# Performance work log

Hardware: AMD Instinct MI355X
Metric: run time of the kernel (lower is better)

## Reference

```python
import jax, jax.numpy as jnp
import numpy as np

B, S = 1, 2048
H, KV, D = 32, 8, 128          # query heads, kv heads, head_size
G = H // KV                     # num_queries_per_kv (GQA group size)
SCALE = 1.0 / float(np.sqrt(D))


def setup_inputs() -> dict:
    key = jax.random.key(0)
    k1, k2, k3 = jax.random.split(key, 3)
    slopes = jnp.asarray(2.0 ** (-8.0 * np.arange(1, H + 1) / H), dtype=jnp.float32)
    return {
        "query": jax.random.normal(k1, (B, S, H * D), dtype=jnp.float32),
        "key": jax.random.normal(k2, (B, S, KV * D), dtype=jnp.float32),
        "value": jax.random.normal(k3, (B, S, KV * D), dtype=jnp.float32),
        "alibi_slopes": slopes,
    }


def reference(query, key, value, alibi_slopes):
    b, s, _ = query.shape
    # [B,S,H*D] -> [B,KV,G,S,D] (GQA unflatten of query heads into kv groups)
    q = query.reshape(b, s, KV, G, D).transpose(0, 2, 3, 1, 4)
    k = key.reshape(b, s, KV, D).transpose(0, 2, 1, 3)      # [B,KV,S,D]
    v = value.reshape(b, s, KV, D).transpose(0, 2, 1, 3)    # [B,KV,S,D]

    # _make_alibi_bias: bias[i,j] = (j - i) * slope_h, then unflatten heads to (KV, G)
    pos = jnp.arange(s)
    rel = (pos[None, :] - pos[:, None]).astype(query.dtype)         # [S,S]
    bias = alibi_slopes[:, None, None] * rel                        # [H,S,S]
    causal = jnp.where(pos[None, :] > pos[:, None], -jnp.inf, 0.0).astype(query.dtype)
    bias = (bias + causal).reshape(KV, G, s, s)                     # [KV,G,S,S]

    # scaled QK^T + bias, softmax, AV (non-fused prompt_attention path)
    scores = jnp.einsum('bkgsd,bktd->bkgst', q * SCALE, k) + bias   # [B,KV,G,S,S]
    probs = jax.nn.softmax(scores, axis=-1)
    out = jnp.einsum('bkgst,bktd->bkgsd', probs, v)                 # [B,KV,G,S,D]
    # flatten (KV,G) -> H and back to [B,S,H*D]
    return out.transpose(0, 3, 1, 2, 4).reshape(b, s, H * D)
```

## Files before the change

kernel.cpp:

```cpp
#include <hip/hip_runtime.h>
#include <hip/hip_bf16.h>

#define S_LEN 2048
#define NHEADS 32
#define NKV 8
#define HD 128
#define QK_SCALE 0.08838834764831845f
#define LOG2E 1.4426950408889634f
#define QK_SCALE2 (QK_SCALE * LOG2E)
#define DTHR 11.5416f

#define BQ 64
#define BK 32
#define NQT (S_LEN / BQ)
#define QSTR (NHEADS * HD)
#define KSTR (NKV * HD)

#define K_STRIDE 136
#define VT_STRIDE 40

typedef __attribute__((ext_vector_type(8))) short bf16x8;
typedef __attribute__((ext_vector_type(4))) float f32x4;
typedef __attribute__((ext_vector_type(4))) unsigned u32x4;

__device__ inline unsigned cvt_pk_bf16(float lo, float hi) {
    unsigned r;
    asm("v_cvt_pk_bf16_f32 %0, %1, %2" : "=v"(r) : "v"(lo), "v"(hi));
    return r;
}
__device__ inline bf16x8 as_bf16x8(u32x4 v) {
    union { u32x4 u; bf16x8 b; } c; c.u = v; return c.b;
}

__global__ __launch_bounds__(256) void attn_fwd(
    const float* __restrict__ Q, const float* __restrict__ K,
    const float* __restrict__ V, const float* __restrict__ SL,
    float* __restrict__ O)
{
    const int bx   = blockIdx.x;
    const int h    = bx & (NHEADS - 1);
    const int qt   = (NQT - 1) - (bx >> 5);
    const int kvh  = h >> 2;
    const float slope  = SL[h];
    const float slope2 = slope * LOG2E;

    const int tid  = threadIdx.x;
    const int lane = tid & 63;
    const int w    = tid >> 6;
    const int l16  = lane & 15;
    const int lq   = lane >> 4;

    __shared__ short Ks[2][BK * K_STRIDE];
    __shared__ short VTs[2][HD * VT_STRIDE];

    const int qrow0 = qt * BQ + w * 16;
    const int q     = qrow0 + l16;

    bf16x8 qf[4];
    {
        const float* qp = Q + (size_t)q * QSTR + h * HD + lq * 8;
        #pragma unroll
        for (int d0 = 0; d0 < 4; ++d0) {
            f32x4 a = *(const f32x4*)(qp + d0 * 32);
            f32x4 b = *(const f32x4*)(qp + d0 * 32 + 4);
            u32x4 t;
            t[0] = cvt_pk_bf16(a[0] * QK_SCALE2, a[1] * QK_SCALE2);
            t[1] = cvt_pk_bf16(a[2] * QK_SCALE2, a[3] * QK_SCALE2);
            t[2] = cvt_pk_bf16(b[0] * QK_SCALE2, b[1] * QK_SCALE2);
            t[3] = cvt_pk_bf16(b[2] * QK_SCALE2, b[3] * QK_SCALE2);
            qf[d0] = as_bf16x8(t);
        }
    }

    f32x4 acc[8];
    #pragma unroll
    for (int t = 0; t < 8; ++t) acc[t] = (f32x4){0.f, 0.f, 0.f, 0.f};
    float m_ = -1e30f, l_ = 0.f;

    const int kv_end = qt * BQ + BQ;
    int kb_start = 0;
    {
        float th = (float)(qt * BQ) - 31.0f - 45.0f / slope;
        int t = (int)floorf(th);
        kb_start = (t < 0) ? 0 : (((t >> 5) + 1) << 5);
    }

    const int sr  = tid >> 4, scc = tid & 15;
    const int vd  = tid & 127, vrb = (tid >> 7) * 8;
    const float* Kbase = K + (size_t)kvh * HD + scc * 8;
    const float* Vbase = V + (size_t)kvh * HD + vd;

    float kr[2][8], vr[2][8];

    auto load_regs = [&](int kb) {
        #pragma unroll
        for (int s = 0; s < 2; ++s) {
            const float* kp = Kbase + (size_t)(kb + sr + s * 16) * KSTR;
            *(f32x4*)&kr[s][0] = *(const f32x4*)kp;
            *(f32x4*)&kr[s][4] = *(const f32x4*)(kp + 4);
        }
        #pragma unroll
        for (int s = 0; s < 2; ++s)
            #pragma unroll
            for (int j = 0; j < 8; ++j)
                vr[s][j] = Vbase[(size_t)(kb + vrb + s * 16 + j) * KSTR];
    };

    auto store_tile = [&](int b) {
        #pragma unroll
        for (int s = 0; s < 2; ++s) {
            u32x4 t;
            t[0] = cvt_pk_bf16(kr[s][0], kr[s][1]);
            t[1] = cvt_pk_bf16(kr[s][2], kr[s][3]);
            t[2] = cvt_pk_bf16(kr[s][4], kr[s][5]);
            t[3] = cvt_pk_bf16(kr[s][6], kr[s][7]);
            *(u32x4*)&Ks[b][(sr + s * 16) * K_STRIDE + scc * 8] = t;
        }
        #pragma unroll
        for (int s = 0; s < 2; ++s) {
            u32x4 t;
            t[0] = cvt_pk_bf16(vr[s][0], vr[s][1]);
            t[1] = cvt_pk_bf16(vr[s][2], vr[s][3]);
            t[2] = cvt_pk_bf16(vr[s][4], vr[s][5]);
            t[3] = cvt_pk_bf16(vr[s][6], vr[s][7]);
            *(u32x4*)&VTs[b][vd * VT_STRIDE + vrb + s * 16] = t;
        }
    };

    load_regs(kb_start);
    store_tile(0);
    int cur = 0;

    const int srcA = l16 + ((lane & 16) << 1);
    const int srcB = srcA + 16;
    const bool lowk = (lq < 2);

    for (int kb = kb_start; kb < kv_end; kb += BK) {
        asm volatile("s_waitcnt lgkmcnt(0)\n\ts_barrier" ::: "memory");

        const bool has_next = (kb + BK) < kv_end;
        if (has_next) load_regs(kb + BK);

        const bool live = (kb <= qrow0 + 15) &&
                          (slope * (float)(qrow0 - kb - 31) < 45.0f);
        if (live) {
            const short* Kc = &Ks[cur][0];
            const short* Vc = &VTs[cur][0];

            f32x4 sc0 = (f32x4){0.f,0.f,0.f,0.f};
            f32x4 sc1 = (f32x4){0.f,0.f,0.f,0.f};
            #pragma unroll
            for (int d0 = 0; d0 < 4; ++d0) {
                bf16x8 kf0 = *(const bf16x8*)&Kc[l16 * K_STRIDE + d0 * 32 + lq * 8];
                bf16x8 kf1 = *(const bf16x8*)&Kc[(16 + l16) * K_STRIDE + d0 * 32 + lq * 8];
                sc0 = __builtin_amdgcn_mfma_f32_16x16x32_bf16(kf0, qf[d0], sc0, 0, 0, 0);
                sc1 = __builtin_amdgcn_mfma_f32_16x16x32_bf16(kf1, qf[d0], sc1, 0, 0, 0);
            }

            const int kq0 = kb + 4 * lq - q;
            float s[8];
            #pragma unroll
            for (int i = 0; i < 4; ++i) {
                int d0i = kq0 + i, d1i = kq0 + 16 + i;
                float b0 = __builtin_fmaf(slope2, (float)d0i, sc0[i]);
                float b1 = __builtin_fmaf(slope2, (float)d1i, sc1[i]);
                s[i]     = (d0i > 0) ? -1e30f : b0;
                s[i + 4] = (d1i > 0) ? -1e30f : b1;
            }

            float rm = fmaxf(fmaxf(fmaxf(s[0], s[1]), fmaxf(s[2], s[3])),
                             fmaxf(fmaxf(s[4], s[5]), fmaxf(s[6], s[7])));
            rm = fmaxf(rm, __shfl_xor(rm, 16));
            rm = fmaxf(rm, __shfl_xor(rm, 32));

            bool need = (rm > m_ + DTHR);
            if (__any(need)) {
                float mn    = need ? rm : m_;
                float alpha = exp2f(m_ - mn);
                m_ = mn;
                l_ *= alpha;
                #pragma unroll
                for (int t = 0; t < 8; ++t) {
                    acc[t][0] *= alpha; acc[t][1] *= alpha;
                    acc[t][2] *= alpha; acc[t][3] *= alpha;
                }
            }

            float p[8];
            #pragma unroll
            for (int j = 0; j < 8; ++j) p[j] = exp2f(s[j] - m_);
            float ts = ((p[0] + p[1]) + (p[2] + p[3])) +
                       ((p[4] + p[5]) + (p[6] + p[7]));
            ts += __shfl_xor(ts, 16);
            ts += __shfl_xor(ts, 32);
            l_ += ts;

            unsigned t0 = cvt_pk_bf16(p[0], p[1]);
            unsigned t1 = cvt_pk_bf16(p[2], p[3]);
            unsigned t2 = cvt_pk_bf16(p[4], p[5]);
            unsigned t3 = cvt_pk_bf16(p[6], p[7]);
            unsigned a0 = __shfl(t0, srcA), c0 = __shfl(t2, srcA);
            unsigned a1 = __shfl(t1, srcA), c1 = __shfl(t3, srcA);
            unsigned a2 = __shfl(t0, srcB), c2 = __shfl(t2, srcB);
            unsigned a3 = __shfl(t1, srcB), c3 = __shfl(t3, srcB);
            u32x4 Bf;
            Bf[0] = lowk ? a0 : c0;
            Bf[1] = lowk ? a1 : c1;
            Bf[2] = lowk ? a2 : c2;
            Bf[3] = lowk ? a3 : c3;
            bf16x8 pf = as_bf16x8(Bf);

            #pragma unroll
            for (int nt = 0; nt < 8; ++nt) {
                bf16x8 vf = *(const bf16x8*)&Vc[(nt * 16 + l16) * VT_STRIDE + lq * 8];
                acc[nt] = __builtin_amdgcn_mfma_f32_16x16x32_bf16(vf, pf, acc[nt], 0, 0, 0);
            }
        }

        if (has_next) store_tile(cur ^ 1);
        cur ^= 1;
    }

    {
        float rl = 1.0f / l_;
        float* op = O + (size_t)q * QSTR + h * HD + 4 * lq;
        #pragma unroll
        for (int nt = 0; nt < 8; ++nt) {
            f32x4 o = acc[nt];
            o[0] *= rl; o[1] *= rl; o[2] *= rl; o[3] *= rl;
            *(f32x4*)(op + nt * 16) = o;
        }
    }
}

extern "C" void kernel_launch(void* const* d_in, const int* in_sizes, int n_in,
                              void* d_out, int out_size, void* d_ws, size_t ws_size,
                              hipStream_t stream) {
    const float* Q  = (const float*)d_in[0];
    const float* K  = (const float*)d_in[1];
    const float* V  = (const float*)d_in[2];
    const float* SL = (const float*)d_in[3];
    float* O = (float*)d_out;

    dim3 grid(NQT * NHEADS);
    dim3 block(256);
    attn_fwd<<<grid, block, 0, stream>>>(Q, K, V, SL, O);
}
```

Measured before the change: 105.7 us.

## Double KV tile to 64 rows with per-half liveness and set wave priority

Raises the KV tile from 32 to 64 keys per iteration, halving the barrier and loop overhead and doing one softmax rescale per 64 keys. Each 32-key half keeps its own ALiBi/causal liveness check. The start position is aligned down to 64, and s_setprio raises priority for blocks with long KV windows. The cost is doubled LDS and staging registers, which may reduce occupancy, plus some wasted loads on dead half-tiles.

Measured after the change: 128.1 us. 21.2% more time.

```diff
diff --git a/kernel.cpp b/kernel.cpp
--- a/kernel.cpp
+++ b/kernel.cpp
@@ -11,13 +11,13 @@
 #define DTHR 11.5416f
 
 #define BQ 64
-#define BK 32
+#define BK 64
 #define NQT (S_LEN / BQ)
 #define QSTR (NHEADS * HD)
 #define KSTR (NKV * HD)
 
 #define K_STRIDE 136
-#define VT_STRIDE 40
+#define VT_STRIDE 72
 
 typedef __attribute__((ext_vector_type(8))) short bf16x8;
 typedef __attribute__((ext_vector_type(4))) float f32x4;
@@ -78,29 +78,34 @@
     float m_ = -1e30f, l_ = 0.f;
 
     const int kv_end = qt * BQ + BQ;
-    int kb_start = 0;
+    int kb0 = 0;
     {
         float th = (float)(qt * BQ) - 31.0f - 45.0f / slope;
         int t = (int)floorf(th);
-        kb_start = (t < 0) ? 0 : (((t >> 5) + 1) << 5);
-    }
+        int kbs = (t < 0) ? 0 : (((t >> 5) + 1) << 5);
+        kb0 = kbs & ~63;
+    }
+
+    const int window = kv_end - kb0;
+    if (window >= 1536)      __builtin_amdgcn_s_setprio(3);
+    else if (window >= 768)  __builtin_amdgcn_s_setprio(2);
 
     const int sr  = tid >> 4, scc = tid & 15;
     const int vd  = tid & 127, vrb = (tid >> 7) * 8;
     const float* Kbase = K + (size_t)kvh * HD + scc * 8;
     const float* Vbase = V + (size_t)kvh * HD + vd;
 
-    float kr[2][8], vr[2][8];
+    float kr[4][8], vr[4][8];
 
     auto load_regs = [&](int kb) {
         #pragma unroll
-        for (int s = 0; s < 2; ++s) {
+        for (int s = 0; s < 4; ++s) {
             const float* kp = Kbase + (size_t)(kb + sr + s * 16) * KSTR;
             *(f32x4*)&kr[s][0] = *(const f32x4*)kp;
             *(f32x4*)&kr[s][4] = *(const f32x4*)(kp + 4);
         }
         #pragma unroll
-        for (int s = 0; s < 2; ++s)
+        for (int s = 0; s < 4; ++s)
             #pragma unroll
             for (int j = 0; j < 8; ++j)
                 vr[s][j] = Vbase[(size_t)(kb + vrb + s * 16 + j) * KSTR];
@@ -108,7 +113,7 @@
 
     auto store_tile = [&](int b) {
         #pragma unroll
-        for (int s = 0; s < 2; ++s) {
+        for (int s = 0; s < 4; ++s) {
             u32x4 t;
             t[0] = cvt_pk_bf16(kr[s][0], kr[s][1]);
             t[1] = cvt_pk_bf16(kr[s][2], kr[s][3]);
@@ -117,7 +122,7 @@
             *(u32x4*)&Ks[b][(sr + s * 16) * K_STRIDE + scc * 8] = t;
         }
         #pragma unroll
-        for (int s = 0; s < 2; ++s) {
+        for (int s = 0; s < 4; ++s) {
             u32x4 t;
             t[0] = cvt_pk_bf16(vr[s][0], vr[s][1]);
             t[1] = cvt_pk_bf16(vr[s][2], vr[s][3]);
@@ -127,7 +132,7 @@
         }
     };
 
-    load_regs(kb_start);
+    load_regs(kb0);
     store_tile(0);
     int cur = 0;
 
@@ -135,41 +140,56 @@
     const int srcB = srcA + 16;
     const bool lowk = (lq < 2);
 
-    for (int kb = kb_start; kb < kv_end; kb += BK) {
+    for (int kb = kb0; kb < kv_end; kb += BK) {
         asm volatile("s_waitcnt lgkmcnt(0)\n\ts_barrier" ::: "memory");
 
         const bool has_next = (kb + BK) < kv_end;
         if (has_next) load_regs(kb + BK);
 
-        const bool live = (kb <= qrow0 + 15) &&
-                          (slope * (float)(qrow0 - kb - 31) < 45.0f);
-        if (live) {
+        bool liveS[2];
+        #pragma unroll
+        for (int c = 0; c < 2; ++c) {
+            const int ks = kb + 32 * c;
+            liveS[c] = (ks <= qrow0 + 15) &&
+                       (slope * (float)(qrow0 - ks - 31) < 45.0f);
+        }
+
+        if (liveS[0] || liveS[1]) {
             const short* Kc = &Ks[cur][0];
             const short* Vc = &VTs[cur][0];
 
-            f32x4 sc0 = (f32x4){0.f,0.f,0.f,0.f};
-            f32x4 sc1 = (f32x4){0.f,0.f,0.f,0.f};
-            #pragma unroll
-            for (int d0 = 0; d0 < 4; ++d0) {
-                bf16x8 kf0 = *(const bf16x8*)&Kc[l16 * K_STRIDE + d0 * 32 + lq * 8];
-                bf16x8 kf1 = *(const bf16x8*)&Kc[(16 + l16) * K_STRIDE + d0 * 32 + lq * 8];
-                sc0 = __builtin_amdgcn_mfma_f32_16x16x32_bf16(kf0, qf[d0], sc0, 0, 0, 0);
-                sc1 = __builtin_amdgcn_mfma_f32_16x16x32_bf16(kf1, qf[d0], sc1, 0, 0, 0);
-            }
-
+            f32x4 sc[4];
+            #pragma unroll
+            for (int g = 0; g < 4; ++g) sc[g] = (f32x4){0.f,0.f,0.f,0.f};
+            #pragma unroll
+            for (int c = 0; c < 2; ++c) {
+                if (!liveS[c]) continue;
+                #pragma unroll
+                for (int d0 = 0; d0 < 4; ++d0) {
+                    bf16x8 kfA = *(const bf16x8*)&Kc[(32*c + l16) * K_STRIDE + d0 * 32 + lq * 8];
+                    bf16x8 kfB = *(const bf16x8*)&Kc[(32*c + 16 + l16) * K_STRIDE + d0 * 32 + lq * 8];
+                    sc[2*c]   = __builtin_amdgcn_mfma_f32_16x16x32_bf16(kfA, qf[d0], sc[2*c],   0, 0, 0);
+                    sc[2*c+1] = __builtin_amdgcn_mfma_f32_16x16x32_bf16(kfB, qf[d0], sc[2*c+1], 0, 0, 0);
+                }
+            }
+
+            float s[16];
             const int kq0 = kb + 4 * lq - q;
-            float s[8];
-            #pragma unroll
-            for (int i = 0; i < 4; ++i) {
-                int d0i = kq0 + i, d1i = kq0 + 16 + i;
-                float b0 = __builtin_fmaf(slope2, (float)d0i, sc0[i]);
-                float b1 = __builtin_fmaf(slope2, (float)d1i, sc1[i]);
-                s[i]     = (d0i > 0) ? -1e30f : b0;
-                s[i + 4] = (d1i > 0) ? -1e30f : b1;
-            }
-
-            float rm = fmaxf(fmaxf(fmaxf(s[0], s[1]), fmaxf(s[2], s[3])),
+            #pragma unroll
+            for (int g = 0; g < 4; ++g) {
+                #pragma unroll
+                for (int i = 0; i < 4; ++i) {
+                    int d = kq0 + 16 * g + i;
+                    float b = __builtin_fmaf(slope2, (float)d, sc[g][i]);
+                    s[4*g + i] = (d > 0) ? -1e30f : b;
+                }
+            }
+
+            float r0 = fmaxf(fmaxf(fmaxf(s[0], s[1]), fmaxf(s[2], s[3])),
                              fmaxf(fmaxf(s[4], s[5]), fmaxf(s[6], s[7])));
+            float r1 = fmaxf(fmaxf(fmaxf(s[8], s[9]), fmaxf(s[10], s[11])),
+                             fmaxf(fmaxf(s[12], s[13]), fmaxf(s[14], s[15])));
+            float rm = fmaxf(r0, r1);
             rm = fmaxf(rm, __shfl_xor(rm, 16));
             rm = fmaxf(rm, __shfl_xor(rm, 32));
 
@@ -186,34 +206,40 @@
                 }
             }
 
-            float p[8];
-            #pragma unroll
-            for (int j = 0; j < 8; ++j) p[j] = exp2f(s[j] - m_);
-            float ts = ((p[0] + p[1]) + (p[2] + p[3])) +
-                       ((p[4] + p[5]) + (p[6] + p[7]));
+            float p[16];
+            #pragma unroll
+            for (int j = 0; j < 16; ++j) p[j] = exp2f(s[j] - m_);
+            float ts = 0.f;
+            #pragma unroll
+            for (int j = 0; j < 16; ++j) ts += p[j];
             ts += __shfl_xor(ts, 16);
             ts += __shfl_xor(ts, 32);
             l_ += ts;
 
-            unsigned t0 = cvt_pk_bf16(p[0], p[1]);
-            unsigned t1 = cvt_pk_bf16(p[2], p[3]);
-            unsigned t2 = cvt_pk_bf16(p[4], p[5]);
-            unsigned t3 = cvt_pk_bf16(p[6], p[7]);
-            unsigned a0 = __shfl(t0, srcA), c0 = __shfl(t2, srcA);
-            unsigned a1 = __shfl(t1, srcA), c1 = __shfl(t3, srcA);
-            unsigned a2 = __shfl(t0, srcB), c2 = __shfl(t2, srcB);
-            unsigned a3 = __shfl(t1, srcB), c3 = __shfl(t3, srcB);
-            u32x4 Bf;
-            Bf[0] = lowk ? a0 : c0;
-            Bf[1] = lowk ? a1 : c1;
-            Bf[2] = lowk ? a2 : c2;
-            Bf[3] = lowk ? a3 : c3;
-            bf16x8 pf = as_bf16x8(Bf);
-
-            #pragma unroll
-            for (int nt = 0; nt < 8; ++nt) {
-                bf16x8 vf = *(const bf16x8*)&Vc[(nt * 16 + l16) * VT_STRIDE + lq * 8];
-                acc[nt] = __builtin_amdgcn_mfma_f32_16x16x32_bf16(vf, pf, acc[nt], 0, 0, 0);
+            #pragma unroll
+            for (int c = 0; c < 2; ++c) {
+                if (!liveS[c]) continue;
+                const float* pc = &p[8 * c];
+                unsigned t0 = cvt_pk_bf16(pc[0], pc[1]);
+                unsigned t1 = cvt_pk_bf16(pc[2], pc[3]);
+                unsigned t2 = cvt_pk_bf16(pc[4], pc[5]);
+                unsigned t3 = cvt_pk_bf16(pc[6], pc[7]);
+                unsigned a0 = __shfl(t0, srcA), c0 = __shfl(t2, srcA);
+                unsigned a1 = __shfl(t1, srcA), c1 = __shfl(t3, srcA);
+                unsigned a2 = __shfl(t0, srcB), c2 = __shfl(t2, srcB);
+                unsigned a3 = __shfl(t1, srcB), c3 = __shfl(t3, srcB);
+                u32x4 Bf;
+                Bf[0] = lowk ? a0 : c0;
+                Bf[1] = lowk ? a1 : c1;
+                Bf[2] = lowk ? a2 : c2;
+                Bf[3] = lowk ? a3 : c3;
+                bf16x8 pf = as_bf16x8(Bf);
+
+                #pragma unroll
+                for (int nt = 0; nt < 8; ++nt) {
+                    bf16x8 vf = *(const bf16x8*)&Vc[(nt * 16 + l16) * VT_STRIDE + 32*c + lq * 8];
+                    acc[nt] = __builtin_amdgcn_mfma_f32_16x16x32_bf16(vf, pf, acc[nt], 0, 0, 0);
+                }
             }
         }
 
```
